# Kernel tuning notes

Measured on AMD Instinct MI355X. Metric: run time of the kernel, lower is better.

Reference implementation:

```python
import jax, jax.numpy as jnp
import numpy as np

N, E, F, H = 8192, 131072, 128, 128
K = N // 2  # pooling ratio = 0.5


def setup_inputs():
    key = jax.random.key(0)
    ks = jax.random.split(key, 16)
    g = lambda i, shape, s: jax.random.normal(ks[i], shape, jnp.float32) * s
    w = 0.1
    return {
        "nodes": g(0, (N, F), 1.0),
        "edges": jax.random.randint(ks[1], (2, E), 0, N, dtype=jnp.int32),
        "batch": jnp.zeros((N,), jnp.int32),
        "w1": g(2, (F, H), w), "b1": jnp.zeros((H,), jnp.float32),
        "w2": g(3, (H, H), w), "b2": jnp.zeros((H,), jnp.float32),
        "w3": g(4, (H, H), w), "b3": jnp.zeros((H,), jnp.float32),
        "w4": g(5, (H, H), w), "b4": jnp.zeros((H,), jnp.float32),
        "w5": g(6, (H, F), w), "b5": jnp.zeros((F,), jnp.float32),
        "wq": g(7, (H, H), w), "bq": jnp.zeros((H,), jnp.float32),
        "att": g(8, (2 * H,), w),
        "lw1": g(9, (H, 1), w), "lb1": jnp.zeros((1,), jnp.float32),
        "lw2": g(10, (H, 1), w), "lw3": g(11, (H, 1), w),
    }


def reference(nodes, edges, batch, w1, b1, w2, b2, w3, b3, w4, b4, w5, b5,
              wq, bq, att, lw1, lb1, lw2, lw3):
    n = nodes.shape[0]
    src, dst = edges[0], edges[1]
    loop = jnp.arange(n, dtype=src.dtype)
    srcl = jnp.concatenate([src, loop])  # edges + self loops
    dstl = jnp.concatenate([dst, loop])
    deg = jax.ops.segment_sum(jnp.ones(srcl.shape[0], nodes.dtype), dstl, n)
    dis = jax.lax.rsqrt(jnp.maximum(deg, 1.0))
    norm = dis[srcl] * dis[dstl]  # GCN symmetric normalization

    def gcn(x, w, b):
        return jax.ops.segment_sum((x @ w)[srcl] * norm[:, None], dstl, n) + b

    h = jnp.tanh(gcn(nodes, w1, b1))
    h = jnp.tanh(gcn(h, w2, b2))

    # ---- ASAP pooling ----
    h_src = h[srcl]
    # cluster query: max over 1-hop neighborhood, then linear
    xq = jax.ops.segment_max(h_src, dstl, n) @ wq + bq
    # edge attention score, softmax per destination (cluster)
    e = jax.nn.leaky_relu(jnp.concatenate([xq[dstl], h_src], axis=-1) @ att, 0.2)
    ee = jnp.exp(e - jax.ops.segment_max(e, dstl, n)[dstl])
    alpha = ee / jax.ops.segment_sum(ee, dstl, n)[dstl]
    cx = jax.ops.segment_sum(h_src * alpha[:, None], dstl, n)  # cluster reps [N,H]
    # LEConv fitness score (out_dim = 1)
    aggr = jax.ops.segment_sum((cx @ lw2)[dstl] - (cx @ lw3)[srcl], dstl, n)
    fit = jax.nn.sigmoid((cx @ lw1 + lb1 + aggr)[:, 0])
    fitk, perm = jax.lax.top_k(fit, K)
    xp = cx[perm] * fitk[:, None]  # pooled node features [K,H]
    # dense assignment matrix S [N,K]: S[i, j] = alpha(i -> perm[j])
    inv = jnp.full((n,), -1, jnp.int32).at[perm].set(jnp.arange(K, dtype=jnp.int32))
    col = inv[dstl]
    valid = col >= 0
    S = jnp.zeros((n, K), nodes.dtype).at[
        srcl, jnp.where(valid, col, 0)].add(jnp.where(valid, alpha, 0.0))
    # dense adjacency (with self loops) and coarsened adjacency Ac = S^T A S
    A = jnp.zeros((n, n), nodes.dtype).at[srcl, dstl].add(1.0)
    Ac = S.T @ (A @ S)  # [K,K]

    # ---- autoencoder reconstruction via bmm with S ----
    x_out = S @ xp               # [N,H]
    adj_out = S @ (Ac @ S.T)     # [N,N]

    x2 = jnp.tanh(gcn(x_out, w3, b3))
    x2 = jnp.tanh(gcn(x2, w4, b4))
    x2 = gcn(x2, w5, b5)
    return x2, adj_out[None]
```

## Files before the change

kernel.cpp:

```cpp
#include <hip/hip_runtime.h>
#include <math.h>

#define NN 8192
#define EE 131072
#define ELn 139264
#define HH 128
#define KK 4096

__device__ __forceinline__ int esrc(const int* __restrict__ edges, int e){ return e < EE ? edges[e] : e - EE; }
__device__ __forceinline__ int edst(const int* __restrict__ edges, int e){ return e < EE ? edges[EE + e] : e - EE; }

__global__ void k_count_indeg(const int* __restrict__ edges, int* __restrict__ deg){
  int e = blockIdx.x*blockDim.x + threadIdx.x;
  if (e < ELn) atomicAdd(&deg[edst(edges,e)], 1);
}
__global__ void k_count_src(const int* __restrict__ edges, int* __restrict__ cnt){
  int e = blockIdx.x*blockDim.x + threadIdx.x;
  if (e < ELn) atomicAdd(&cnt[esrc(edges,e)], 1);
}

__global__ void k_dis(const int* __restrict__ deg, float* __restrict__ dis){
  int v = blockIdx.x*blockDim.x + threadIdx.x;
  if (v < NN){ float d = (float)deg[v]; d = d < 1.0f ? 1.0f : d; dis[v] = 1.0f/sqrtf(d); }
}

template<int IPT>
__global__ __launch_bounds__(1024) void k_scan(const int* __restrict__ cnt, int* __restrict__ rowptr, int* __restrict__ cur){
  __shared__ int part[1024];
  int tid = threadIdx.x;
  int base = tid*IPT;
  int loc[IPT]; int s=0;
  #pragma unroll
  for (int i=0;i<IPT;i++) loc[i]=cnt[base+i];
  #pragma unroll
  for (int i=0;i<IPT;i++){ int t=loc[i]; loc[i]=s; s+=t; }
  part[tid]=s;
  __syncthreads();
  for (int off=1; off<1024; off<<=1){
    int v = (tid>=off)? part[tid-off] : 0;
    __syncthreads();
    part[tid]+=v;
    __syncthreads();
  }
  int cb = part[tid]-s;
  #pragma unroll
  for (int i=0;i<IPT;i++){ int r=cb+loc[i]; rowptr[base+i]=r; cur[base+i]=r; }
  if (tid==1023) rowptr[1024*IPT]=part[1023];
}

__global__ void k_fill_dst(const int* __restrict__ edges, int* __restrict__ cur,
                           int* __restrict__ delist, int* __restrict__ desrc){
  int e = blockIdx.x*blockDim.x + threadIdx.x;
  if (e < ELn){
    int v = edst(edges,e);
    int pos = atomicAdd(&cur[v],1);
    delist[pos] = e;
    desrc[pos]  = esrc(edges,e);
  }
}
__global__ void k_fill_src(const int* __restrict__ edges, int* __restrict__ cur, int* __restrict__ esdst){
  int e = blockIdx.x*blockDim.x + threadIdx.x;
  if (e < ELn){
    int u = esrc(edges,e);
    int pos = atomicAdd(&cur[u],1);
    esdst[pos] = edst(edges,e);
  }
}

__global__ __launch_bounds__(256) void k_gemm8(const float* __restrict__ x, const float* __restrict__ W,
     const float* __restrict__ bias, const float* __restrict__ scale, float* __restrict__ y){
  __shared__ float xl[8*HH];
  int tid = threadIdx.x;
  int r0 = blockIdx.x*8;
  {
    int row = tid>>5, col = (tid&31)*4;
    *(float4*)&xl[row*HH+col] = *(const float4*)&x[(size_t)(r0+row)*HH+col];
  }
  __syncthreads();
  int c = tid & 127, h = tid>>7;
  float acc0=0,acc1=0,acc2=0,acc3=0;
  const float* xr = &xl[h*4*HH];
  #pragma unroll 8
  for (int k=0;k<HH;++k){
    float wv = W[k*HH+c];
    acc0 += xr[k]*wv;
    acc1 += xr[HH+k]*wv;
    acc2 += xr[2*HH+k]*wv;
    acc3 += xr[3*HH+k]*wv;
  }
  float b = bias ? bias[c] : 0.0f;
  float r[4] = {acc0+b, acc1+b, acc2+b, acc3+b};
  #pragma unroll
  for (int j=0;j<4;j++){
    int rr = r0 + h*4 + j;
    float v = r[j];
    if (scale) v *= scale[rr];
    y[(size_t)rr*HH + c] = v;
  }
}

template<int TANH>
__global__ void k_gcn(const float* __restrict__ y, const int* __restrict__ desrc,
    const int* __restrict__ drowptr, const float* __restrict__ dis,
    const float* __restrict__ bias, float* __restrict__ out){
  int v = blockIdx.x, f = threadIdx.x;
  int beg = drowptr[v], end = drowptr[v+1];
  float acc = 0.0f;
  for (int i=beg;i<end;++i){
    int u = desrc[i];
    acc += y[(size_t)u*HH+f];
  }
  acc = acc*dis[v] + bias[f];
  if (TANH) acc = tanhf(acc);
  out[(size_t)v*HH+f] = acc;
}

__global__ void k_segmax(const float* __restrict__ h, const int* __restrict__ desrc,
    const int* __restrict__ drowptr, float* __restrict__ out){
  int v = blockIdx.x, f = threadIdx.x;
  int beg = drowptr[v], end = drowptr[v+1];
  float m = -3.4e38f;
  for (int i=beg;i<end;++i){
    int u = desrc[i];
    m = fmaxf(m, h[(size_t)u*HH+f]);
  }
  out[(size_t)v*HH+f] = m;
}

__global__ void k_aqah(const float* __restrict__ xq, const float* __restrict__ h,
                       const float* __restrict__ att, float* __restrict__ aq, float* __restrict__ ah){
  int v = blockIdx.x, t = threadIdx.x;
  float a1 = xq[(size_t)v*HH+t]*att[t];
  float a2 = h[(size_t)v*HH+t]*att[HH+t];
  #pragma unroll
  for (int off=32; off; off>>=1){ a1 += __shfl_down(a1,off); a2 += __shfl_down(a2,off); }
  __shared__ float s1[2], s2[2];
  if ((t&63)==0){ s1[t>>6]=a1; s2[t>>6]=a2; }
  __syncthreads();
  if (t==0){ aq[v]=s1[0]+s1[1]; ah[v]=s2[0]+s2[1]; }
}

__global__ __launch_bounds__(256) void k_alpha(const int* __restrict__ delist, const int* __restrict__ desrc,
    const int* __restrict__ drowptr, const float* __restrict__ aq, const float* __restrict__ ah,
    float* __restrict__ alpha){
  int v = blockIdx.x*4 + (threadIdx.x>>6);
  int lane = threadIdx.x & 63;
  int beg = drowptr[v], end = drowptr[v+1];
  float aqv = aq[v];
  float m = -3.4e38f;
  for (int i=beg+lane; i<end; i+=64){
    float s = aqv + ah[desrc[i]];
    s = s > 0.0f ? s : 0.2f*s;
    m = fmaxf(m, s);
  }
  #pragma unroll
  for (int off=32; off; off>>=1) m = fmaxf(m, __shfl_xor(m, off));
  float den = 0.0f;
  for (int i=beg+lane; i<end; i+=64){
    float s = aqv + ah[desrc[i]];
    s = s > 0.0f ? s : 0.2f*s;
    den += expf(s - m);
  }
  #pragma unroll
  for (int off=32; off; off>>=1) den += __shfl_xor(den, off);
  float inv = 1.0f/den;
  for (int i=beg+lane; i<end; i+=64){
    float s = aqv + ah[desrc[i]];
    s = s > 0.0f ? s : 0.2f*s;
    alpha[delist[i]] = expf(s - m)*inv;
  }
}

__global__ void k_cx(const float* __restrict__ h, const int* __restrict__ delist,
    const int* __restrict__ desrc, const int* __restrict__ drowptr,
    const float* __restrict__ alpha, float* __restrict__ cx){
  int v = blockIdx.x, f = threadIdx.x;
  int beg = drowptr[v], end = drowptr[v+1];
  float acc = 0.0f;
  for (int i=beg;i<end;++i){
    acc += alpha[delist[i]]*h[(size_t)desrc[i]*HH+f];
  }
  cx[(size_t)v*HH+f] = acc;
}

__global__ void k_le(const float* __restrict__ cx, const float* __restrict__ lw1,
                     const float* __restrict__ lw2, const float* __restrict__ lw3,
                     float* __restrict__ l1, float* __restrict__ l2, float* __restrict__ l3){
  int v = blockIdx.x, t = threadIdx.x;
  float cv = cx[(size_t)v*HH+t];
  float a = cv*lw1[t], b = cv*lw2[t], c = cv*lw3[t];
  #pragma unroll
  for (int off=32; off; off>>=1){ a += __shfl_down(a,off); b += __shfl_down(b,off); c += __shfl_down(c,off); }
  __shared__ float sa[2], sb[2], sc[2];
  if ((t&63)==0){ sa[t>>6]=a; sb[t>>6]=b; sc[t>>6]=c; }
  __syncthreads();
  if (t==0){ l1[v]=sa[0]+sa[1]; l2[v]=sb[0]+sb[1]; l3[v]=sc[0]+sc[1]; }
}

__global__ __launch_bounds__(256) void k_fit(const int* __restrict__ desrc, const int* __restrict__ drowptr,
    const float* __restrict__ l1, const float* __restrict__ l2, const float* __restrict__ l3,
    const float* __restrict__ lb1, float* __restrict__ fit){
  int v = blockIdx.x*4 + (threadIdx.x>>6);
  int lane = threadIdx.x & 63;
  int beg = drowptr[v], end = drowptr[v+1];
  float s = 0.0f;
  for (int i=beg+lane;i<end;i+=64) s += l3[desrc[i]];
  #pragma unroll
  for (int off=32; off; off>>=1) s += __shfl_xor(s, off);
  if (lane==0){
    float degf = (float)(end-beg);
    float x = l1[v] + lb1[0] + degf*l2[v] - s;
    fit[v] = 1.0f/(1.0f+expf(-x));
  }
}

__global__ __launch_bounds__(1024) void k_topk(const float* __restrict__ fit, int* __restrict__ perm,
                        float* __restrict__ fitk, int* __restrict__ inv){
  __shared__ unsigned long long keys[NN];
  int tid = threadIdx.x;
  for (int i=tid;i<NN;i+=1024){
    unsigned u = __float_as_uint(fit[i]);
    unsigned mono = (u>>31) ? ~u : (u|0x80000000u);
    keys[i] = ((unsigned long long)(~mono)<<32) | (unsigned)i;
    inv[i] = -1;
  }
  __syncthreads();
  for (int k=2;k<=NN;k<<=1)
    for (int j=k>>1;j>0;j>>=1){
      for (int t=tid;t<NN;t+=1024){
        int ixj = t^j;
        if (ixj > t){
          bool up = ((t&k)==0);
          unsigned long long a = keys[t], b = keys[ixj];
          if (up ? (a>b) : (a<b)){ keys[t]=b; keys[ixj]=a; }
        }
      }
      __syncthreads();
    }
  for (int i=tid;i<KK;i+=1024){
    int idx = (int)(keys[i] & 0xffffffffu);
    perm[i]=idx; fitk[i]=fit[idx]; inv[idx]=i;
  }
}

__global__ void k_xp(const float* __restrict__ cx, const int* __restrict__ perm,
                     const float* __restrict__ fitk, float* __restrict__ xp){
  int j = blockIdx.x, f = threadIdx.x;
  xp[(size_t)j*HH+f] = cx[(size_t)perm[j]*HH+f]*fitk[j];
}

__global__ void k_scnt(const int* __restrict__ edges, const int* __restrict__ inv, int* __restrict__ scnt){
  int e = blockIdx.x*blockDim.x + threadIdx.x;
  if (e < ELn && inv[edst(edges,e)] >= 0) atomicAdd(&scnt[esrc(edges,e)],1);
}

__global__ void k_fill_s(const int* __restrict__ edges, const int* __restrict__ inv,
                         const float* __restrict__ alpha, int* __restrict__ scur,
                         int2* __restrict__ spair, int* __restrict__ srow_of){
  int e = blockIdx.x*blockDim.x + threadIdx.x;
  if (e < ELn){
    int j = inv[edst(edges,e)];
    if (j >= 0){
      int u = esrc(edges,e);
      int pos = atomicAdd(&scur[u],1);
      spair[pos] = make_int2(j, __float_as_int(alpha[e]));
      srow_of[pos] = u;
    }
  }
}

__global__ void k_col_cnt(const int2* __restrict__ spair, const int* __restrict__ srowptr, int* __restrict__ ccnt){
  int i = blockIdx.x*blockDim.x + threadIdx.x;
  if (i < srowptr[NN]) atomicAdd(&ccnt[spair[i].x], 1);
}
__global__ void k_col_fill(const int2* __restrict__ spair, const int* __restrict__ srow_of,
                           const int* __restrict__ srowptr, int* __restrict__ ccur,
                           int* __restrict__ colu, float* __restrict__ cval){
  int i = blockIdx.x*blockDim.x + threadIdx.x;
  if (i < srowptr[NN]){
    int2 p = spair[i];
    int pos = atomicAdd(&ccur[p.x], 1);
    colu[pos] = srow_of[i];
    cval[pos] = __int_as_float(p.y);
  }
}

__global__ void k_xout(const float* __restrict__ xp, const int* __restrict__ srowptr,
                       const int2* __restrict__ spair, float* __restrict__ xout){
  int u = blockIdx.x, f = threadIdx.x;
  int beg = srowptr[u], end = srowptr[u+1];
  float acc = 0.0f;
  for (int i=beg;i<end;++i){
    int2 p = spair[i];
    acc += __int_as_float(p.y)*xp[(size_t)p.x*HH+f];
  }
  xout[(size_t)u*HH+f] = acc;
}

#define ACCAP 2048
__global__ __launch_bounds__(256) void k_ac2(const int* __restrict__ cptr, const int* __restrict__ colu,
     const float* __restrict__ cval, const int* __restrict__ esptr, const int* __restrict__ esdst,
     const int* __restrict__ srowptr, const int2* __restrict__ spair, float* __restrict__ Ac){
  __shared__ float row[KK];
  __shared__ int   lv[ACCAP];
  __shared__ float lval[ACCAP];
  int tid = threadIdx.x;
  int p = blockIdx.x;
  for (int i=tid;i<KK;i+=256) row[i]=0.0f;
  int cb = cptr[p], ce = cptr[p+1];
  int base = 0;
  int j = cb;
  while (true){
    while (j < ce){
      int u = colu[j]; float val = cval[j];
      int eb = esptr[u], d = esptr[u+1]-eb;
      if (base + d > ACCAP) break;
      for (int t=tid; t<d; t+=256){ lv[base+t]=esdst[eb+t]; lval[base+t]=val; }
      base += d; ++j;
    }
    __syncthreads();
    for (int i=tid;i<base;i+=256){
      int v = lv[i]; float a = lval[i];
      int sb = srowptr[v], se = srowptr[v+1];
      for (int k=sb;k<se;++k){
        int2 q = spair[k];
        atomicAdd(&row[q.x], a*__int_as_float(q.y));
      }
    }
    __syncthreads();
    base = 0;
    if (j >= ce) break;
  }
  for (int i=tid;i<KK;i+=256) Ac[(size_t)p*KK+i] = row[i];
}

__global__ __launch_bounds__(1024) void k_adj(const float* __restrict__ Ac, const int* __restrict__ srowptr,
      const int2* __restrict__ spair, float* __restrict__ adj){
  __shared__ float Uf[KK*4];
  int tid = threadIdx.x;
  int u0 = blockIdx.x*4;
  float acc[4][4];
  #pragma unroll
  for (int jj=0;jj<4;jj++)
    #pragma unroll
    for (int g=0;g<4;g++) acc[jj][g]=0.f;
  int q0 = tid*4;
  #pragma unroll
  for (int g=0; g<4; ++g){
    int beg = srowptr[u0+g], end = srowptr[u0+g+1];
    for (int i=beg;i<end;++i){
      int2 pr = spair[i];
      float a = __int_as_float(pr.y);
      float4 av = *(const float4*)(Ac + (size_t)pr.x*KK + q0);
      acc[0][g] += a*av.x; acc[1][g] += a*av.y; acc[2][g] += a*av.z; acc[3][g] += a*av.w;
    }
  }
  #pragma unroll
  for (int jj=0;jj<4;jj++){
    *(float4*)&Uf[(q0+jj)*4] = make_float4(acc[jj][0],acc[jj][1],acc[jj][2],acc[jj][3]);
  }
  __syncthreads();
  for (int wb=0; wb<NN; wb+=1024){
    int w = wb + tid;
    int beg = srowptr[w], end = srowptr[w+1];
    float r0=0,r1=0,r2=0,r3=0;
    for (int i=beg;i<end;++i){
      int2 p = spair[i];
      float b = __int_as_float(p.y);
      float4 u4 = *(const float4*)&Uf[p.x*4];
      r0 += b*u4.x; r1 += b*u4.y; r2 += b*u4.z; r3 += b*u4.w;
    }
    adj[(size_t)(u0+0)*NN + w] = r0;
    adj[(size_t)(u0+1)*NN + w] = r1;
    adj[(size_t)(u0+2)*NN + w] = r2;
    adj[(size_t)(u0+3)*NN + w] = r3;
  }
}

extern "C" void kernel_launch(void* const* d_in, const int* in_sizes, int n_in,
                              void* d_out, int out_size, void* d_ws, size_t ws_size,
                              hipStream_t stream){
  const float* nodes = (const float*)d_in[0];
  const int*   edges = (const int*)d_in[1];
  const float* w1=(const float*)d_in[3];  const float* b1=(const float*)d_in[4];
  const float* w2=(const float*)d_in[5];  const float* b2=(const float*)d_in[6];
  const float* w3=(const float*)d_in[7];  const float* b3=(const float*)d_in[8];
  const float* w4=(const float*)d_in[9];  const float* b4=(const float*)d_in[10];
  const float* w5=(const float*)d_in[11]; const float* b5=(const float*)d_in[12];
  const float* wq=(const float*)d_in[13]; const float* bq=(const float*)d_in[14];
  const float* att=(const float*)d_in[15];
  const float* lw1=(const float*)d_in[16]; const float* lb1=(const float*)d_in[17];
  const float* lw2=(const float*)d_in[18]; const float* lw3=(const float*)d_in[19];

  char* ws = (char*)d_ws;
  size_t off = 0;
  auto take = [&](size_t bytes)->char*{
    char* p = ws + off;
    off = (off + bytes + 255) & ~(size_t)255;
    return p;
  };
  int*   deg     = (int*)  take((size_t)NN*4);
  float* dis     = (float*)take((size_t)NN*4);
  int*   drowptr = (int*)  take((size_t)(NN+1)*4);
  int*   dcur    = (int*)  take((size_t)NN*4);
  int*   delist  = (int*)  take((size_t)ELn*4);
  float* alpha   = (float*)take((size_t)ELn*4);
  float* aq      = (float*)take((size_t)NN*4);
  float* ah      = (float*)take((size_t)NN*4);
  float* l1      = (float*)take((size_t)NN*4);
  float* l2      = (float*)take((size_t)NN*4);
  float* l3      = (float*)take((size_t)NN*4);
  float* fit     = (float*)take((size_t)NN*4);
  int*   perm    = (int*)  take((size_t)KK*4);
  float* fitk    = (float*)take((size_t)KK*4);
  int*   inv     = (int*)  take((size_t)NN*4);
  int*   scnt    = (int*)  take((size_t)NN*4);
  int*   srowptr = (int*)  take((size_t)(NN+1)*4);
  int*   scur    = (int*)  take((size_t)NN*4);
  int2*  spair   = (int2*) take((size_t)ELn*8);
  int*   ecnt    = (int*)  take((size_t)NN*4);
  int*   esptr   = (int*)  take((size_t)(NN+1)*4);
  int*   ecur    = (int*)  take((size_t)NN*4);
  int*   ccnt    = (int*)  take((size_t)KK*4);
  int*   cptr    = (int*)  take((size_t)(KK+1)*4);
  int*   ccur    = (int*)  take((size_t)KK*4);
  float* Ac      = (float*)take((size_t)KK*KK*4);
  (void)ws_size; (void)in_sizes; (void)n_in; (void)out_size;

  float* out_x2 = (float*)d_out;
  float* adj    = (float*)d_out + (size_t)NN*HH;
  float* BA = adj + 0*(size_t)NN*HH;
  float* BB = adj + 1*(size_t)NN*HH;
  float* BC = adj + 2*(size_t)NN*HH;
  float* BD = adj + 3*(size_t)NN*HH;
  float* BE = adj + 4*(size_t)NN*HH;
  float* BF = adj + 5*(size_t)NN*HH;
  float* BG = adj + 6*(size_t)NN*HH;
  float* xp = adj + 7*(size_t)NN*HH;
  char*  sc2 = (char*)(adj + 8*(size_t)NN*HH);
  int*   desrc   = (int*)  sc2;                       sc2 += (size_t)ELn*4;
  int*   esdst   = (int*)  sc2;                       sc2 += (size_t)ELn*4;
  int*   srow_of = (int*)  sc2;                       sc2 += (size_t)ELn*4;
  int*   colu    = (int*)  sc2;                       sc2 += (size_t)ELn*4;
  float* cval    = (float*)sc2;                       sc2 += (size_t)ELn*4;

  const int EB = ELn/256;

  hipMemsetAsync(deg, 0, (size_t)NN*4, stream);
  hipMemsetAsync(ecnt, 0, (size_t)NN*4, stream);
  k_count_indeg<<<EB,256,0,stream>>>(edges,deg);
  k_count_src<<<EB,256,0,stream>>>(edges,ecnt);
  k_dis<<<NN/256,256,0,stream>>>(deg,dis);
  k_scan<8><<<1,1024,0,stream>>>(deg,drowptr,dcur);
  k_fill_dst<<<EB,256,0,stream>>>(edges,dcur,delist,desrc);
  k_scan<8><<<1,1024,0,stream>>>(ecnt,esptr,ecur);
  k_fill_src<<<EB,256,0,stream>>>(edges,ecur,esdst);

  k_gemm8<<<NN/8,256,0,stream>>>(nodes,w1,nullptr,dis,BA);
  k_gcn<1><<<NN,128,0,stream>>>(BA,desrc,drowptr,dis,b1,BB);
  k_gemm8<<<NN/8,256,0,stream>>>(BB,w2,nullptr,dis,BA);
  k_gcn<1><<<NN,128,0,stream>>>(BA,desrc,drowptr,dis,b2,BC);

  k_segmax<<<NN,128,0,stream>>>(BC,desrc,drowptr,BD);
  k_gemm8<<<NN/8,256,0,stream>>>(BD,wq,bq,nullptr,BE);
  k_aqah<<<NN,128,0,stream>>>(BE,BC,att,aq,ah);
  k_alpha<<<NN/4,256,0,stream>>>(delist,desrc,drowptr,aq,ah,alpha);
  k_cx<<<NN,128,0,stream>>>(BC,delist,desrc,drowptr,alpha,BF);
  k_le<<<NN,128,0,stream>>>(BF,lw1,lw2,lw3,l1,l2,l3);
  k_fit<<<NN/4,256,0,stream>>>(desrc,drowptr,l1,l2,l3,lb1,fit);
  k_topk<<<1,1024,0,stream>>>(fit,perm,fitk,inv);
  k_xp<<<KK,128,0,stream>>>(BF,perm,fitk,xp);

  hipMemsetAsync(scnt, 0, (size_t)NN*4, stream);
  k_scnt<<<EB,256,0,stream>>>(edges,inv,scnt);
  k_scan<8><<<1,1024,0,stream>>>(scnt,srowptr,scur);
  k_fill_s<<<EB,256,0,stream>>>(edges,inv,alpha,scur,spair,srow_of);
  hipMemsetAsync(ccnt, 0, (size_t)KK*4, stream);
  k_col_cnt<<<EB,256,0,stream>>>(spair,srowptr,ccnt);
  k_scan<4><<<1,1024,0,stream>>>(ccnt,cptr,ccur);
  k_col_fill<<<EB,256,0,stream>>>(spair,srow_of,srowptr,ccur,colu,cval);

  k_xout<<<NN,128,0,stream>>>(xp,srowptr,spair,BG);
  k_gemm8<<<NN/8,256,0,stream>>>(BG,w3,nullptr,dis,BA);
  k_gcn<1><<<NN,128,0,stream>>>(BA,desrc,drowptr,dis,b3,BB);
  k_gemm8<<<NN/8,256,0,stream>>>(BB,w4,nullptr,dis,BA);
  k_gcn<1><<<NN,128,0,stream>>>(BA,desrc,drowptr,dis,b4,BD);
  k_gemm8<<<NN/8,256,0,stream>>>(BD,w5,nullptr,dis,BA);
  k_gcn<0><<<NN,128,0,stream>>>(BA,desrc,drowptr,dis,b5,out_x2);

  k_ac2<<<KK,256,0,stream>>>(cptr,colu,cval,esptr,esdst,srowptr,spair,Ac);
  k_adj<<<NN/4,1024,0,stream>>>(Ac,srowptr,spair,adj);
}
```

Before: 1.209 ms.

## Fuse GCN aggregation with weight GEMM and widen adj reconstruction tile

```diff
diff --git a/kernel.cpp b/kernel.cpp
--- a/kernel.cpp
+++ b/kernel.cpp
@@ -10,13 +10,12 @@
 __device__ __forceinline__ int esrc(const int* __restrict__ edges, int e){ return e < EE ? edges[e] : e - EE; }
 __device__ __forceinline__ int edst(const int* __restrict__ edges, int e){ return e < EE ? edges[EE + e] : e - EE; }
 
-__global__ void k_count_indeg(const int* __restrict__ edges, int* __restrict__ deg){
+__global__ void k_count(const int* __restrict__ edges, int* __restrict__ indeg, int* __restrict__ outdeg){
   int e = blockIdx.x*blockDim.x + threadIdx.x;
-  if (e < ELn) atomicAdd(&deg[edst(edges,e)], 1);
-}
-__global__ void k_count_src(const int* __restrict__ edges, int* __restrict__ cnt){
-  int e = blockIdx.x*blockDim.x + threadIdx.x;
-  if (e < ELn) atomicAdd(&cnt[esrc(edges,e)], 1);
+  if (e < ELn){
+    atomicAdd(&indeg[edst(edges,e)], 1);
+    atomicAdd(&outdeg[esrc(edges,e)], 1);
+  }
 }
 
 __global__ void k_dis(const int* __restrict__ deg, float* __restrict__ dis){
@@ -67,8 +66,51 @@
   }
 }
 
+template<int TANH>
+__global__ __launch_bounds__(256) void k_layer(const float* __restrict__ x,
+    const int* __restrict__ desrc, const int* __restrict__ drowptr,
+    const float* __restrict__ dis, const float* __restrict__ W,
+    const float* __restrict__ bias, float* __restrict__ out){
+  __shared__ float agg[8][HH];
+  int tid = threadIdx.x;
+  int r0 = blockIdx.x*8;
+  int wv = tid>>6, lane = tid&63;
+  for (int rr=wv; rr<8; rr+=4){
+    int v = r0+rr;
+    int beg = drowptr[v], end = drowptr[v+1];
+    float ax=0.f, ay=0.f;
+    for (int i=beg;i<end;++i){
+      int u = desrc[i];
+      float du = dis[u];
+      float2 xv = *(const float2*)&x[(size_t)u*HH + lane*2];
+      ax += du*xv.x; ay += du*xv.y;
+    }
+    float dv = dis[v];
+    *(float2*)&agg[rr][lane*2] = make_float2(ax*dv, ay*dv);
+  }
+  __syncthreads();
+  int c = tid&127, h = tid>>7;
+  float a0=0,a1=0,a2=0,a3=0;
+  #pragma unroll 4
+  for (int k=0;k<HH;++k){
+    float wv_ = W[k*HH+c];
+    a0 += agg[h*4+0][k]*wv_;
+    a1 += agg[h*4+1][k]*wv_;
+    a2 += agg[h*4+2][k]*wv_;
+    a3 += agg[h*4+3][k]*wv_;
+  }
+  float b = bias[c];
+  float r[4]={a0+b,a1+b,a2+b,a3+b};
+  #pragma unroll
+  for (int j=0;j<4;j++){
+    float v = r[j];
+    if (TANH) v = tanhf(v);
+    out[(size_t)(r0+h*4+j)*HH + c] = v;
+  }
+}
+
 __global__ __launch_bounds__(256) void k_gemm8(const float* __restrict__ x, const float* __restrict__ W,
-     const float* __restrict__ bias, const float* __restrict__ scale, float* __restrict__ y){
+     const float* __restrict__ bias, float* __restrict__ y){
   __shared__ float xl[8*HH];
   int tid = threadIdx.x;
   int r0 = blockIdx.x*8;
@@ -88,31 +130,11 @@
     acc2 += xr[2*HH+k]*wv;
     acc3 += xr[3*HH+k]*wv;
   }
-  float b = bias ? bias[c] : 0.0f;
-  float r[4] = {acc0+b, acc1+b, acc2+b, acc3+b};
-  #pragma unroll
-  for (int j=0;j<4;j++){
-    int rr = r0 + h*4 + j;
-    float v = r[j];
-    if (scale) v *= scale[rr];
-    y[(size_t)rr*HH + c] = v;
-  }
-}
-
-template<int TANH>
-__global__ void k_gcn(const float* __restrict__ y, const int* __restrict__ desrc,
-    const int* __restrict__ drowptr, const float* __restrict__ dis,
-    const float* __restrict__ bias, float* __restrict__ out){
-  int v = blockIdx.x, f = threadIdx.x;
-  int beg = drowptr[v], end = drowptr[v+1];
-  float acc = 0.0f;
-  for (int i=beg;i<end;++i){
-    int u = desrc[i];
-    acc += y[(size_t)u*HH+f];
-  }
-  acc = acc*dis[v] + bias[f];
-  if (TANH) acc = tanhf(acc);
-  out[(size_t)v*HH+f] = acc;
+  float b = bias[c];
+  y[(size_t)(r0+h*4+0)*HH + c] = acc0+b;
+  y[(size_t)(r0+h*4+1)*HH + c] = acc1+b;
+  y[(size_t)(r0+h*4+2)*HH + c] = acc2+b;
+  y[(size_t)(r0+h*4+3)*HH + c] = acc3+b;
 }
 
 __global__ void k_segmax(const float* __restrict__ h, const int* __restrict__ desrc,
@@ -336,44 +358,38 @@
 
 __global__ __launch_bounds__(1024) void k_adj(const float* __restrict__ Ac, const int* __restrict__ srowptr,
       const int2* __restrict__ spair, float* __restrict__ adj){
-  __shared__ float Uf[KK*4];
+  __shared__ float U[8*KK];
   int tid = threadIdx.x;
-  int u0 = blockIdx.x*4;
-  float acc[4][4];
-  #pragma unroll
-  for (int jj=0;jj<4;jj++)
-    #pragma unroll
-    for (int g=0;g<4;g++) acc[jj][g]=0.f;
-  int q0 = tid*4;
-  #pragma unroll
-  for (int g=0; g<4; ++g){
+  int u0 = blockIdx.x*8;
+  #pragma unroll
+  for (int g=0; g<8; ++g){
     int beg = srowptr[u0+g], end = srowptr[u0+g+1];
+    float ux=0.f, uy=0.f, uz=0.f, uw=0.f;
     for (int i=beg;i<end;++i){
       int2 pr = spair[i];
       float a = __int_as_float(pr.y);
-      float4 av = *(const float4*)(Ac + (size_t)pr.x*KK + q0);
-      acc[0][g] += a*av.x; acc[1][g] += a*av.y; acc[2][g] += a*av.z; acc[3][g] += a*av.w;
-    }
-  }
-  #pragma unroll
-  for (int jj=0;jj<4;jj++){
-    *(float4*)&Uf[(q0+jj)*4] = make_float4(acc[jj][0],acc[jj][1],acc[jj][2],acc[jj][3]);
+      float4 av = *(const float4*)(Ac + (size_t)pr.x*KK + 4*tid);
+      ux += a*av.x; uy += a*av.y; uz += a*av.z; uw += a*av.w;
+    }
+    *(float4*)&U[g*KK + 4*tid] = make_float4(ux,uy,uz,uw);
   }
   __syncthreads();
   for (int wb=0; wb<NN; wb+=1024){
     int w = wb + tid;
     int beg = srowptr[w], end = srowptr[w+1];
-    float r0=0,r1=0,r2=0,r3=0;
+    float acc[8];
+    #pragma unroll
+    for (int g=0;g<8;g++) acc[g]=0.f;
     for (int i=beg;i<end;++i){
       int2 p = spair[i];
       float b = __int_as_float(p.y);
-      float4 u4 = *(const float4*)&Uf[p.x*4];
-      r0 += b*u4.x; r1 += b*u4.y; r2 += b*u4.z; r3 += b*u4.w;
-    }
-    adj[(size_t)(u0+0)*NN + w] = r0;
-    adj[(size_t)(u0+1)*NN + w] = r1;
-    adj[(size_t)(u0+2)*NN + w] = r2;
-    adj[(size_t)(u0+3)*NN + w] = r3;
+      int q = p.x;
+      #pragma unroll
+      for (int g=0;g<8;g++) acc[g] += b*U[g*KK+q];
+    }
+    #pragma unroll
+    for (int g=0;g<8;g++)
+      __builtin_nontemporal_store(acc[g], &adj[(size_t)(u0+g)*NN + w]);
   }
 }
 
@@ -429,15 +445,14 @@
 
   float* out_x2 = (float*)d_out;
   float* adj    = (float*)d_out + (size_t)NN*HH;
-  float* BA = adj + 0*(size_t)NN*HH;
-  float* BB = adj + 1*(size_t)NN*HH;
-  float* BC = adj + 2*(size_t)NN*HH;
-  float* BD = adj + 3*(size_t)NN*HH;
-  float* BE = adj + 4*(size_t)NN*HH;
-  float* BF = adj + 5*(size_t)NN*HH;
-  float* BG = adj + 6*(size_t)NN*HH;
-  float* xp = adj + 7*(size_t)NN*HH;
-  char*  sc2 = (char*)(adj + 8*(size_t)NN*HH);
+  float* BB = adj + 0*(size_t)NN*HH;
+  float* BC = adj + 1*(size_t)NN*HH;
+  float* BD = adj + 2*(size_t)NN*HH;
+  float* BE = adj + 3*(size_t)NN*HH;
+  float* BF = adj + 4*(size_t)NN*HH;
+  float* BG = adj + 5*(size_t)NN*HH;
+  float* xp = adj + 6*(size_t)NN*HH;
+  char*  sc2 = (char*)(adj + 7*(size_t)NN*HH);
   int*   desrc   = (int*)  sc2;                       sc2 += (size_t)ELn*4;
   int*   esdst   = (int*)  sc2;                       sc2 += (size_t)ELn*4;
   int*   srow_of = (int*)  sc2;                       sc2 += (size_t)ELn*4;
@@ -448,21 +463,18 @@
 
   hipMemsetAsync(deg, 0, (size_t)NN*4, stream);
   hipMemsetAsync(ecnt, 0, (size_t)NN*4, stream);
-  k_count_indeg<<<EB,256,0,stream>>>(edges,deg);
-  k_count_src<<<EB,256,0,stream>>>(edges,ecnt);
+  k_count<<<EB,256,0,stream>>>(edges,deg,ecnt);
   k_dis<<<NN/256,256,0,stream>>>(deg,dis);
   k_scan<8><<<1,1024,0,stream>>>(deg,drowptr,dcur);
   k_fill_dst<<<EB,256,0,stream>>>(edges,dcur,delist,desrc);
   k_scan<8><<<1,1024,0,stream>>>(ecnt,esptr,ecur);
   k_fill_src<<<EB,256,0,stream>>>(edges,ecur,esdst);
 
-  k_gemm8<<<NN/8,256,0,stream>>>(nodes,w1,nullptr,dis,BA);
-  k_gcn<1><<<NN,128,0,stream>>>(BA,desrc,drowptr,dis,b1,BB);
-  k_gemm8<<<NN/8,256,0,stream>>>(BB,w2,nullptr,dis,BA);
-  k_gcn<1><<<NN,128,0,stream>>>(BA,desrc,drowptr,dis,b2,BC);
+  k_layer<1><<<NN/8,256,0,stream>>>(nodes,desrc,drowptr,dis,w1,b1,BB);
+  k_layer<1><<<NN/8,256,0,stream>>>(BB,desrc,drowptr,dis,w2,b2,BC);
 
   k_segmax<<<NN,128,0,stream>>>(BC,desrc,drowptr,BD);
-  k_gemm8<<<NN/8,256,0,stream>>>(BD,wq,bq,nullptr,BE);
+  k_gemm8<<<NN/8,256,0,stream>>>(BD,wq,bq,BE);
   k_aqah<<<NN,128,0,stream>>>(BE,BC,att,aq,ah);
   k_alpha<<<NN/4,256,0,stream>>>(delist,desrc,drowptr,aq,ah,alpha);
   k_cx<<<NN,128,0,stream>>>(BC,delist,desrc,drowptr,alpha,BF);
@@ -481,13 +493,10 @@
   k_col_fill<<<EB,256,0,stream>>>(spair,srow_of,srowptr,ccur,colu,cval);
 
   k_xout<<<NN,128,0,stream>>>(xp,srowptr,spair,BG);
-  k_gemm8<<<NN/8,256,0,stream>>>(BG,w3,nullptr,dis,BA);
-  k_gcn<1><<<NN,128,0,stream>>>(BA,desrc,drowptr,dis,b3,BB);
-  k_gemm8<<<NN/8,256,0,stream>>>(BB,w4,nullptr,dis,BA);
-  k_gcn<1><<<NN,128,0,stream>>>(BA,desrc,drowptr,dis,b4,BD);
-  k_gemm8<<<NN/8,256,0,stream>>>(BD,w5,nullptr,dis,BA);
-  k_gcn<0><<<NN,128,0,stream>>>(BA,desrc,drowptr,dis,b5,out_x2);
+  k_layer<1><<<NN/8,256,0,stream>>>(BG,desrc,drowptr,dis,w3,b3,BB);
+  k_layer<1><<<NN/8,256,0,stream>>>(BB,desrc,drowptr,dis,w4,b4,BD);
+  k_layer<0><<<NN/8,256,0,stream>>>(BD,desrc,drowptr,dis,w5,b5,out_x2);
 
   k_ac2<<<KK,256,0,stream>>>(cptr,colu,cval,esptr,esdst,srowptr,spair,Ac);
-  k_adj<<<NN/4,1024,0,stream>>>(Ac,srowptr,spair,adj);
-}
+  k_adj<<<NN/8,1024,0,stream>>>(Ac,srowptr,spair,adj);
+}
```

Result: faster. 1.118 ms (-7.5%).
